# Kernel tuning notes

Measured on AMD Instinct MI355X. Metric: run time of the kernel, lower is better.

Reference implementation:

```python
import jax, jax.numpy as jnp
import numpy as np

NUM_HEADS = 16
D_MODEL = 1024
ROPE_THETA = 10000.0


def rope_cos_sin(H, W, head_dim, theta):
    # SAM2/SAM3 axial RoPE: first half of complex dims encode x, second half y.
    n = H * W
    t = jnp.arange(n)
    tx = (t % W).astype(jnp.float32)
    ty = (t // W).astype(jnp.float32)
    # freqs: 1 / theta^(arange(0, dim, 4)[:dim//4] / dim)
    exps = jnp.arange(0, head_dim, 4)[: head_dim // 4].astype(jnp.float32) / head_dim
    freqs = 1.0 / (theta ** exps)  # (head_dim//4,)
    ang = jnp.concatenate([tx[:, None] * freqs, ty[:, None] * freqs], axis=-1)  # (N, head_dim//2)
    return jnp.cos(ang), jnp.sin(ang)


def apply_rope(x, cos, sin):
    # x: (B, nh, N, D); pairs of features treated as complex numbers
    B, nh, N, D = x.shape
    xr = x.reshape(B, nh, N, D // 2, 2)
    xe, xo = xr[..., 0], xr[..., 1]
    oe = xe * cos - xo * sin
    oo = xe * sin + xo * cos
    return jnp.stack([oe, oo], axis=-1).reshape(B, nh, N, D)


def setup_inputs() -> dict:
    key = jax.random.key(0)
    ks = jax.random.split(key, 12)
    C = D_MODEL
    s = 1.0 / np.sqrt(C)
    inp = {
        "q": jax.random.normal(ks[0], (2, 2048, C), dtype=jnp.float32),
        "k": jax.random.normal(ks[1], (2, 2112, C), dtype=jnp.float32),
        "v": jax.random.normal(ks[2], (2, 2112, C), dtype=jnp.float32),
        "Wq": jax.random.normal(ks[3], (C, C), dtype=jnp.float32) * s,
        "bq": jax.random.normal(ks[4], (C,), dtype=jnp.float32) * s,
        "Wk": jax.random.normal(ks[5], (C, C), dtype=jnp.float32) * s,
        "bk": jax.random.normal(ks[6], (C,), dtype=jnp.float32) * s,
        "Wv": jax.random.normal(ks[7], (C, C), dtype=jnp.float32) * s,
        "bv": jax.random.normal(ks[8], (C,), dtype=jnp.float32) * s,
        "Wo": jax.random.normal(ks[9], (C, C), dtype=jnp.float32) * s,
        "bo": jax.random.normal(ks[10], (C,), dtype=jnp.float32) * s,
        "q_h": 32,
        "q_w": 64,
        "num_final_k_to_exclude": 64,
    }
    return inp


def reference(q, k, v, Wq, bq, Wk, bk, Wv, bv, Wo, bo, q_h, q_w, num_final_k_to_exclude):
    B, Nq, C = q.shape
    Nk = k.shape[1]
    nh = NUM_HEADS
    d = C // nh
    # QKV projections -> (B, nh, N, d)
    qh = (q @ Wq + bq).reshape(B, Nq, nh, d).transpose(0, 2, 1, 3)
    kh = (k @ Wk + bk).reshape(B, Nk, nh, d).transpose(0, 2, 1, 3)
    vh = (v @ Wv + bv).reshape(B, Nk, nh, d).transpose(0, 2, 1, 3)
    # RoPE on q and on first num_k_keep keys (exclude trailing pointer tokens)
    n_keep = Nk - num_final_k_to_exclude  # == q_h * q_w == Nq here
    cos, sin = rope_cos_sin(q_h, q_w, d, ROPE_THETA)
    qh = apply_rope(qh, cos, sin)
    k_rot = apply_rope(kh[:, :, :n_keep], cos, sin)
    kh = jnp.concatenate([k_rot, kh[:, :, n_keep:]], axis=2)
    # scaled dot-product attention
    scale = 1.0 / np.sqrt(d)
    scores = jnp.einsum("bhqd,bhkd->bhqk", qh, kh) * scale
    probs = jax.nn.softmax(scores, axis=-1)
    attn = jnp.einsum("bhqk,bhkd->bhqd", probs, vh)
    out = attn.transpose(0, 2, 1, 3).reshape(B, Nq, C)
    return out @ Wo + bo
```

## Files before the change

### kernel.cpp

```cpp
#include <hip/hip_runtime.h>

#define B_ 2
#define NQ 2048
#define NK 2112
#define CD 1024
#define NH 16
#define HD 64

typedef unsigned short u16;
typedef unsigned int u32;
typedef __attribute__((ext_vector_type(8))) __bf16 bf16x8;
typedef __attribute__((ext_vector_type(4))) float f32x4;

#define GPTR(p) ((const __attribute__((address_space(1))) void*)(p))
#define LPTR(p) ((__attribute__((address_space(3))) void*)(p))
#define GLL16(g, l) __builtin_amdgcn_global_load_lds(GPTR(g), LPTR(l), 16, 0, 0)

__device__ __forceinline__ u16 f2bf(float f) {
  u32 u = __float_as_uint(f);
  u32 r = u + 0x7fffu + ((u >> 16) & 1u);
  return (u16)(r >> 16);
}
__device__ __forceinline__ float bf2f(u16 h) { return __uint_as_float(((u32)h) << 16); }

__global__ void cvt3_kernel(const float* __restrict__ q, const float* __restrict__ k,
                            const float* __restrict__ v, u16* __restrict__ qb,
                            u16* __restrict__ kb, u16* __restrict__ vb) {
  int z = blockIdx.y;
  const float* src = (z == 0) ? q : (z == 1) ? k : v;
  u16* dst = (z == 0) ? qb : (z == 1) ? kb : vb;
  int n4 = (z == 0) ? (B_ * NQ * CD / 4) : (B_ * NK * CD / 4);
  int i = blockIdx.x * 256 + threadIdx.x;
  if (i >= n4) return;
  float4 vv = ((const float4*)src)[i];
  ushort4 o;
  o.x = f2bf(vv.x); o.y = f2bf(vv.y); o.z = f2bf(vv.z); o.w = f2bf(vv.w);
  ((ushort4*)dst)[i] = o;
}

__global__ void wtrans_kernel(const float* __restrict__ W0, const float* __restrict__ W1,
                              const float* __restrict__ W2, const float* __restrict__ W3,
                              u16* __restrict__ T0, u16* __restrict__ T1,
                              u16* __restrict__ T2, u16* __restrict__ T3) {
  const float* src; u16* dst;
  switch (blockIdx.z) {
    case 0: src = W0; dst = T0; break;
    case 1: src = W1; dst = T1; break;
    case 2: src = W2; dst = T2; break;
    default: src = W3; dst = T3; break;
  }
  __shared__ u16 tile[32][33];
  int t = threadIdx.x;
  int r0 = blockIdx.y * 32, c0 = blockIdx.x * 32;
  int row = t >> 3, c4 = (t & 7) * 4;
  float4 v = *(const float4*)&src[(r0 + row) * 1024 + c0 + c4];
  tile[row][c4 + 0] = f2bf(v.x);
  tile[row][c4 + 1] = f2bf(v.y);
  tile[row][c4 + 2] = f2bf(v.z);
  tile[row][c4 + 3] = f2bf(v.w);
  __syncthreads();
  ushort4 o;
  o.x = tile[c4 + 0][row];
  o.y = tile[c4 + 1][row];
  o.z = tile[c4 + 2][row];
  o.w = tile[c4 + 3][row];
  *(ushort4*)&dst[(c0 + row) * 1024 + r0 + c4] = o;
}

#define SC 0.18033688011112042f

__global__ __launch_bounds__(256, 2) void gemm_qkv(
    const u16* __restrict__ qb, const u16* __restrict__ kb, const u16* __restrict__ vb,
    const u16* __restrict__ wqt, const u16* __restrict__ wkt, const u16* __restrict__ wvt,
    const float* __restrict__ bq, const float* __restrict__ bk, const float* __restrict__ bv,
    u16* __restrict__ Qh, u16* __restrict__ Kh, u16* __restrict__ Vt) {
  const int z = blockIdx.z;
  if (z == 0 && blockIdx.y >= 32) return;
  const u16* A = (z == 0) ? qb : (z == 1) ? kb : vb;
  const u16* Bt = (z == 0) ? wqt : (z == 1) ? wkt : wvt;
  const float* bias = (z == 0) ? bq : (z == 1) ? bk : bv;
  const int batch_rows = (z == 0) ? NQ : NK;

  __shared__ u16 As[128 * 32];
  __shared__ u16 Bs[128 * 32];
  const int t = threadIdx.x;
  const int lane = t & 63, w = t >> 6;
  const int lc = lane & 15, lq = lane >> 4;
  const int m0 = blockIdx.y * 128, n0 = blockIdx.x * 128;
  const int wm = (w >> 1) * 64, wn = (w & 1) * 64;
  f32x4 acc[4][4] = {};
  const u16* ga = A + (m0 + (t >> 2)) * 1024 + (t & 3) * 8;
  const u16* gb = Bt + (n0 + (t >> 2)) * 1024 + (t & 3) * 8;
  char* lA = (char*)As + w * 1024;
  char* lB = (char*)Bs + w * 1024;
  for (int k0 = 0; k0 < 1024; k0 += 32) {
    if (k0) __syncthreads();
    GLL16(ga + k0, lA);
    GLL16(ga + 64 * 1024 + k0, lA + 4096);
    GLL16(gb + k0, lB);
    GLL16(gb + 64 * 1024 + k0, lB + 4096);
    __syncthreads();
    bf16x8 af[4], bf[4];
#pragma unroll
    for (int i = 0; i < 4; ++i) {
      af[i] = *(const bf16x8*)&As[(wm + i * 16 + lc) * 32 + lq * 8];
      bf[i] = *(const bf16x8*)&Bs[(wn + i * 16 + lc) * 32 + lq * 8];
    }
#pragma unroll
    for (int mi = 0; mi < 4; ++mi)
#pragma unroll
      for (int ni = 0; ni < 4; ++ni)
        acc[mi][ni] = __builtin_amdgcn_mfma_f32_16x16x32_bf16(af[mi], bf[ni], acc[mi][ni], 0, 0, 0);
  }
#pragma unroll
  for (int mi = 0; mi < 4; ++mi) {
#pragma unroll
    for (int ni = 0; ni < 4; ++ni) {
      int col = n0 + wn + ni * 16 + lc;
      float bv_ = bias[col];
      int j = (col >> 1) & 31;
      bool jlow = j < 16;
      float freq = exp2f((float)(jlow ? j : j - 16) * -0.8304820237f);
#pragma unroll
      for (int r = 0; r < 4; ++r) {
        int row = m0 + wm + mi * 16 + lq * 4 + r;
        float v = acc[mi][ni][r] + bv_;
        if (z < 2) {
          int bb = row >= batch_rows ? 1 : 0;
          int tok = row - bb * batch_rows;
          float p = __shfl_xor(v, 1, 64);
          float ov = v;
          if (tok < 2048) {
            float pos = jlow ? (float)(tok & 63) : (float)(tok >> 6);
            float s, c;
            __sincosf(pos * freq, &s, &c);
            ov = ((col & 1) == 0) ? (v * c - p * s) : (p * s + v * c);
          }
          if (z == 0) ov *= SC;
          ((z == 0) ? Qh : Kh)[row * 1024 + col] = f2bf(ov);
        } else {
          int bb = row >= NK ? 1 : 0;
          int tok = row - bb * NK;
          int h = col >> 6, dd = col & 63;
          Vt[((bb * NH + h) * HD + dd) * NK + tok] = f2bf(v);
        }
      }
    }
  }
}

__global__ __launch_bounds__(256, 2) void gemm_o(const u16* __restrict__ A,
                                                 const u16* __restrict__ Bt,
                                                 const float* __restrict__ bias,
                                                 float* __restrict__ Cout) {
  __shared__ u16 As[128 * 32];
  __shared__ u16 Bs[128 * 32];
  const int t = threadIdx.x;
  const int lane = t & 63, w = t >> 6;
  const int lc = lane & 15, lq = lane >> 4;
  const int m0 = blockIdx.y * 128, n0 = blockIdx.x * 128;
  const int wm = (w >> 1) * 64, wn = (w & 1) * 64;
  f32x4 acc[4][4] = {};
  const u16* ga = A + (m0 + (t >> 2)) * 1024 + (t & 3) * 8;
  const u16* gb = Bt + (n0 + (t >> 2)) * 1024 + (t & 3) * 8;
  char* lA = (char*)As + w * 1024;
  char* lB = (char*)Bs + w * 1024;
  for (int k0 = 0; k0 < 1024; k0 += 32) {
    if (k0) __syncthreads();
    GLL16(ga + k0, lA);
    GLL16(ga + 64 * 1024 + k0, lA + 4096);
    GLL16(gb + k0, lB);
    GLL16(gb + 64 * 1024 + k0, lB + 4096);
    __syncthreads();
    bf16x8 af[4], bf[4];
#pragma unroll
    for (int i = 0; i < 4; ++i) {
      af[i] = *(const bf16x8*)&As[(wm + i * 16 + lc) * 32 + lq * 8];
      bf[i] = *(const bf16x8*)&Bs[(wn + i * 16 + lc) * 32 + lq * 8];
    }
#pragma unroll
    for (int mi = 0; mi < 4; ++mi)
#pragma unroll
      for (int ni = 0; ni < 4; ++ni)
        acc[mi][ni] = __builtin_amdgcn_mfma_f32_16x16x32_bf16(af[mi], bf[ni], acc[mi][ni], 0, 0, 0);
  }
#pragma unroll
  for (int mi = 0; mi < 4; ++mi)
#pragma unroll
    for (int ni = 0; ni < 4; ++ni) {
      int col = n0 + wn + ni * 16 + lc;
      float bv = bias[col];
#pragma unroll
      for (int r = 0; r < 4; ++r) {
        int row = m0 + wm + mi * 16 + lq * 4 + r;
        Cout[row * 1024 + col] = acc[mi][ni][r] + bv;
      }
    }
}

#define LSTR 72
__global__ __launch_bounds__(256, 2) void attn_kernel(const u16* __restrict__ Qh,
                                                      const u16* __restrict__ Kh,
                                                      const u16* __restrict__ Vt,
                                                      u16* __restrict__ AO) {
  __shared__ u16 QPs[128 * LSTR];
  __shared__ u16 Ks[64 * LSTR];
  __shared__ u16 Vs[64 * LSTR];
  const int t = threadIdx.x;
  const int lane = t & 63, w = t >> 6;
  const int lc = lane & 15, lq = lane >> 4;
  const int rr = lane >> 3, s = lane & 7;
  const int qt = blockIdx.x, h = blockIdx.y, b = blockIdx.z;

  {
    const u16* gq = Qh + (b * NQ + qt * 128 + w * 32 + rr) * CD + h * HD + s * 8;
    u16* lqp = &QPs[(w * 32 + rr) * LSTR + s * 8];
#pragma unroll
    for (int i = 0; i < 4; ++i)
      *(uint4*)(lqp + i * 8 * LSTR) = *(const uint4*)(gq + i * 8 * CD);
  }
  bf16x8 qf[2][2];
#pragma unroll
  for (int ni = 0; ni < 2; ++ni)
#pragma unroll
    for (int kk = 0; kk < 2; ++kk)
      qf[ni][kk] = *(const bf16x8*)&QPs[(w * 32 + ni * 16 + lc) * LSTR + kk * 32 + lq * 8];

  bf16x8 ones;
  {
    u32* op = (u32*)&ones;
    op[0] = op[1] = op[2] = op[3] = 0x3F803F80u;
  }

  const u16* gK = Kh + (b * NK + w * 16 + rr) * CD + h * HD + s * 8;
  const u16* gV = Vt + ((b * NH + h) * HD + w * 16 + rr) * NK + s * 8;
  uint4 kreg0, kreg1, vreg0, vreg1;
  kreg0 = *(const uint4*)(gK);
  kreg1 = *(const uint4*)(gK + 8 * CD);
  vreg0 = *(const uint4*)(gV);
  vreg1 = *(const uint4*)(gV + 8 * NK);

  f32x4 oacc[2][4] = {};
  f32x4 lacc[2] = {};

  for (int j0 = 0; j0 < NK; j0 += 64) {
    __syncthreads();
    *(uint4*)&Ks[(w * 16 + rr) * LSTR + s * 8] = kreg0;
    *(uint4*)&Ks[(w * 16 + 8 + rr) * LSTR + s * 8] = kreg1;
    *(uint4*)&Vs[(w * 16 + rr) * LSTR + s * 8] = vreg0;
    *(uint4*)&Vs[(w * 16 + 8 + rr) * LSTR + s * 8] = vreg1;
    __syncthreads();
    if (j0 + 64 < NK) {
      kreg0 = *(const uint4*)(gK + (j0 + 64) * CD);
      kreg1 = *(const uint4*)(gK + (j0 + 64) * CD + 8 * CD);
      vreg0 = *(const uint4*)(gV + j0 + 64);
      vreg1 = *(const uint4*)(gV + 8 * NK + j0 + 64);
    }

    f32x4 st[2][4] = {};
#pragma unroll
    for (int mi = 0; mi < 4; ++mi) {
      bf16x8 k0f = *(const bf16x8*)&Ks[(mi * 16 + lc) * LSTR + lq * 8];
      bf16x8 k1f = *(const bf16x8*)&Ks[(mi * 16 + lc) * LSTR + 32 + lq * 8];
#pragma unroll
      for (int ni = 0; ni < 2; ++ni) {
        st[ni][mi] = __builtin_amdgcn_mfma_f32_16x16x32_bf16(k0f, qf[ni][0], st[ni][mi], 0, 0, 0);
        st[ni][mi] = __builtin_amdgcn_mfma_f32_16x16x32_bf16(k1f, qf[ni][1], st[ni][mi], 0, 0, 0);
      }
    }
#pragma unroll
    for (int ni = 0; ni < 2; ++ni)
#pragma unroll
      for (int mi = 0; mi < 4; ++mi) {
        u32 e0 = __float_as_uint(__builtin_amdgcn_exp2f(st[ni][mi][0])) + 0x8000u;
        u32 e1 = __float_as_uint(__builtin_amdgcn_exp2f(st[ni][mi][1])) + 0x8000u;
        u32 e2 = __float_as_uint(__builtin_amdgcn_exp2f(st[ni][mi][2])) + 0x8000u;
        u32 e3 = __float_as_uint(__builtin_amdgcn_exp2f(st[ni][mi][3])) + 0x8000u;
        uint2 pk;
        pk.x = __builtin_amdgcn_perm(e1, e0, 0x07060302u);
        pk.y = __builtin_amdgcn_perm(e3, e2, 0x07060302u);
        *(uint2*)&QPs[(w * 32 + ni * 16 + lc) * LSTR + mi * 16 + lq * 4] = pk;
      }
#pragma unroll
    for (int kc = 0; kc < 2; ++kc) {
      bf16x8 pf[2], vf[4];
#pragma unroll
      for (int ni = 0; ni < 2; ++ni)
        pf[ni] = *(const bf16x8*)&QPs[(w * 32 + ni * 16 + lc) * LSTR + kc * 32 + lq * 8];
#pragma unroll
      for (int di = 0; di < 4; ++di)
        vf[di] = *(const bf16x8*)&Vs[(di * 16 + lc) * LSTR + kc * 32 + lq * 8];
#pragma unroll
      for (int ni = 0; ni < 2; ++ni) {
#pragma unroll
        for (int di = 0; di < 4; ++di)
          oacc[ni][di] = __builtin_amdgcn_mfma_f32_16x16x32_bf16(pf[ni], vf[di], oacc[ni][di], 0, 0, 0);
        lacc[ni] = __builtin_amdgcn_mfma_f32_16x16x32_bf16(pf[ni], ones, lacc[ni], 0, 0, 0);
      }
    }
  }
#pragma unroll
  for (int ni = 0; ni < 2; ++ni)
#pragma unroll
    for (int r = 0; r < 4; ++r) {
      float inv = 1.0f / lacc[ni][r];
#pragma unroll
      for (int di = 0; di < 4; ++di) {
        int row = qt * 128 + w * 32 + ni * 16 + lq * 4 + r;
        int col = h * HD + di * 16 + lc;
        AO[(b * NQ + row) * CD + col] = f2bf(oacc[ni][di][r] * inv);
      }
    }
}

extern "C" void kernel_launch(void* const* d_in, const int* in_sizes, int n_in,
                              void* d_out, int out_size, void* d_ws, size_t ws_size,
                              hipStream_t stream) {
  const float* q  = (const float*)d_in[0];
  const float* k  = (const float*)d_in[1];
  const float* v  = (const float*)d_in[2];
  const float* Wq = (const float*)d_in[3];
  const float* bq = (const float*)d_in[4];
  const float* Wk = (const float*)d_in[5];
  const float* bk = (const float*)d_in[6];
  const float* Wv = (const float*)d_in[7];
  const float* bv = (const float*)d_in[8];
  const float* Wo = (const float*)d_in[9];
  const float* bo = (const float*)d_in[10];

  char* ws = (char*)d_ws;
  size_t off = 0;
  auto alloc = [&](size_t bytes) {
    char* p = ws + off;
    off += (bytes + 255) & ~(size_t)255;
    return p;
  };
  u16* qb  = (u16*)alloc((size_t)B_ * NQ * CD * 2);
  u16* kb  = (u16*)alloc((size_t)B_ * NK * CD * 2);
  u16* vb  = (u16*)alloc((size_t)B_ * NK * CD * 2);
  u16* wqt = (u16*)alloc((size_t)CD * CD * 2);
  u16* wkt = (u16*)alloc((size_t)CD * CD * 2);
  u16* wvt = (u16*)alloc((size_t)CD * CD * 2);
  u16* wot = (u16*)alloc((size_t)CD * CD * 2);
  u16* Qh  = (u16*)alloc((size_t)B_ * NQ * CD * 2);
  u16* Kh  = (u16*)alloc((size_t)B_ * NK * CD * 2);
  u16* Vt  = (u16*)alloc((size_t)B_ * NK * CD * 2);
  u16* AO  = (u16*)alloc((size_t)B_ * NQ * CD * 2);

  cvt3_kernel<<<dim3(4224, 3), 256, 0, stream>>>(q, k, v, qb, kb, vb);
  wtrans_kernel<<<dim3(32, 32, 4), 256, 0, stream>>>(Wq, Wk, Wv, Wo, wqt, wkt, wvt, wot);
  gemm_qkv<<<dim3(8, 33, 3), 256, 0, stream>>>(qb, kb, vb, wqt, wkt, wvt, bq, bk, bv, Qh, Kh, Vt);
  attn_kernel<<<dim3(16, NH, B_), 256, 0, stream>>>(Qh, Kh, Vt, AO);
  gemm_o<<<dim3(8, 32), 256, 0, stream>>>(AO, wot, bo, (float*)d_out);
}
```

Before: 262.9 us.

## Merge prep kernels, swap MFMA operands for vectorized epilogue stores, shrink O-proj tile

Fuses the activation conversion and weight transpose into one prep launch. In the Q/K projection it swaps the MFMA operands so each lane holds four consecutive columns, which lets the RoPE epilogue run without shuffles and write packed 8-byte stores. The V epilogue writes four consecutive tokens per store into the transposed layout. The output projection uses 128x64 tiles, doubling the grid, with float4 stores. This cuts launch overhead and scattered 2-byte writes, at the cost of more branching and a smaller per-block reuse in the O GEMM.

After: 261.3 us. About the same (-0.6%).

```diff
diff --git a/kernel.cpp b/kernel.cpp
--- a/kernel.cpp
+++ b/kernel.cpp
@@ -23,66 +23,67 @@
 }
 __device__ __forceinline__ float bf2f(u16 h) { return __uint_as_float(((u32)h) << 16); }
 
-__global__ void cvt3_kernel(const float* __restrict__ q, const float* __restrict__ k,
+#define SC 0.18033688011112042f
+#define NEGL2T 0.8304820237f
+#define FSTEP 0.5623413252f
+
+__global__ void prep_kernel(const float* __restrict__ q, const float* __restrict__ k,
                             const float* __restrict__ v, u16* __restrict__ qb,
-                            u16* __restrict__ kb, u16* __restrict__ vb) {
-  int z = blockIdx.y;
-  const float* src = (z == 0) ? q : (z == 1) ? k : v;
-  u16* dst = (z == 0) ? qb : (z == 1) ? kb : vb;
-  int n4 = (z == 0) ? (B_ * NQ * CD / 4) : (B_ * NK * CD / 4);
-  int i = blockIdx.x * 256 + threadIdx.x;
-  if (i >= n4) return;
-  float4 vv = ((const float4*)src)[i];
-  ushort4 o;
-  o.x = f2bf(vv.x); o.y = f2bf(vv.y); o.z = f2bf(vv.z); o.w = f2bf(vv.w);
-  ((ushort4*)dst)[i] = o;
-}
-
-__global__ void wtrans_kernel(const float* __restrict__ W0, const float* __restrict__ W1,
-                              const float* __restrict__ W2, const float* __restrict__ W3,
-                              u16* __restrict__ T0, u16* __restrict__ T1,
-                              u16* __restrict__ T2, u16* __restrict__ T3) {
-  const float* src; u16* dst;
-  switch (blockIdx.z) {
-    case 0: src = W0; dst = T0; break;
-    case 1: src = W1; dst = T1; break;
-    case 2: src = W2; dst = T2; break;
-    default: src = W3; dst = T3; break;
-  }
+                            u16* __restrict__ kb, u16* __restrict__ vb,
+                            const float* __restrict__ W0, const float* __restrict__ W1,
+                            const float* __restrict__ W2, const float* __restrict__ W3,
+                            u16* __restrict__ T0, u16* __restrict__ T1,
+                            u16* __restrict__ T2, u16* __restrict__ T3) {
   __shared__ u16 tile[32][33];
+  int y = blockIdx.y;
   int t = threadIdx.x;
-  int r0 = blockIdx.y * 32, c0 = blockIdx.x * 32;
-  int row = t >> 3, c4 = (t & 7) * 4;
-  float4 v = *(const float4*)&src[(r0 + row) * 1024 + c0 + c4];
-  tile[row][c4 + 0] = f2bf(v.x);
-  tile[row][c4 + 1] = f2bf(v.y);
-  tile[row][c4 + 2] = f2bf(v.z);
-  tile[row][c4 + 3] = f2bf(v.w);
-  __syncthreads();
-  ushort4 o;
-  o.x = tile[c4 + 0][row];
-  o.y = tile[c4 + 1][row];
-  o.z = tile[c4 + 2][row];
-  o.w = tile[c4 + 3][row];
-  *(ushort4*)&dst[(c0 + row) * 1024 + r0 + c4] = o;
-}
-
-#define SC 0.18033688011112042f
+  if (y < 3) {
+    const float* src = (y == 0) ? q : (y == 1) ? k : v;
+    u16* dst = (y == 0) ? qb : (y == 1) ? kb : vb;
+    int n4 = (y == 0) ? (B_ * NQ * CD / 4) : (B_ * NK * CD / 4);
+    int i = blockIdx.x * 256 + t;
+    if (i >= n4) return;
+    float4 vv = ((const float4*)src)[i];
+    ushort4 o;
+    o.x = f2bf(vv.x); o.y = f2bf(vv.y); o.z = f2bf(vv.z); o.w = f2bf(vv.w);
+    ((ushort4*)dst)[i] = o;
+  } else {
+    int x = blockIdx.x;
+    if (x >= 4096) return;
+    int which = x >> 10, xy = x & 1023;
+    const float* src = (which == 0) ? W0 : (which == 1) ? W1 : (which == 2) ? W2 : W3;
+    u16* dst = (which == 0) ? T0 : (which == 1) ? T1 : (which == 2) ? T2 : T3;
+    int r0 = (xy >> 5) * 32, c0 = (xy & 31) * 32;
+    int row = t >> 3, c4 = (t & 7) * 4;
+    float4 vv = *(const float4*)&src[(r0 + row) * 1024 + c0 + c4];
+    tile[row][c4 + 0] = f2bf(vv.x);
+    tile[row][c4 + 1] = f2bf(vv.y);
+    tile[row][c4 + 2] = f2bf(vv.z);
+    tile[row][c4 + 3] = f2bf(vv.w);
+    __syncthreads();
+    ushort4 o;
+    o.x = tile[c4 + 0][row];
+    o.y = tile[c4 + 1][row];
+    o.z = tile[c4 + 2][row];
+    o.w = tile[c4 + 3][row];
+    *(ushort4*)&dst[(c0 + row) * 1024 + r0 + c4] = o;
+  }
+}
 
 __global__ __launch_bounds__(256, 2) void gemm_qkv(
     const u16* __restrict__ qb, const u16* __restrict__ kb, const u16* __restrict__ vb,
     const u16* __restrict__ wqt, const u16* __restrict__ wkt, const u16* __restrict__ wvt,
     const float* __restrict__ bq, const float* __restrict__ bk, const float* __restrict__ bv,
     u16* __restrict__ Qh, u16* __restrict__ Kh, u16* __restrict__ Vt) {
+  __shared__ u16 As[128 * 32];
+  __shared__ u16 Bs[128 * 32];
   const int z = blockIdx.z;
   if (z == 0 && blockIdx.y >= 32) return;
   const u16* A = (z == 0) ? qb : (z == 1) ? kb : vb;
   const u16* Bt = (z == 0) ? wqt : (z == 1) ? wkt : wvt;
   const float* bias = (z == 0) ? bq : (z == 1) ? bk : bv;
-  const int batch_rows = (z == 0) ? NQ : NK;
-
-  __shared__ u16 As[128 * 32];
-  __shared__ u16 Bs[128 * 32];
+  const int BR = (z == 0) ? NQ : NK;
+
   const int t = threadIdx.x;
   const int lane = t & 63, w = t >> 6;
   const int lc = lane & 15, lq = lane >> 4;
@@ -93,6 +94,7 @@
   const u16* gb = Bt + (n0 + (t >> 2)) * 1024 + (t & 3) * 8;
   char* lA = (char*)As + w * 1024;
   char* lB = (char*)Bs + w * 1024;
+  const bool swap = (z < 2);
   for (int k0 = 0; k0 < 1024; k0 += 32) {
     if (k0) __syncthreads();
     GLL16(ga + k0, lA);
@@ -106,44 +108,78 @@
       af[i] = *(const bf16x8*)&As[(wm + i * 16 + lc) * 32 + lq * 8];
       bf[i] = *(const bf16x8*)&Bs[(wn + i * 16 + lc) * 32 + lq * 8];
     }
-#pragma unroll
-    for (int mi = 0; mi < 4; ++mi)
-#pragma unroll
-      for (int ni = 0; ni < 4; ++ni)
-        acc[mi][ni] = __builtin_amdgcn_mfma_f32_16x16x32_bf16(af[mi], bf[ni], acc[mi][ni], 0, 0, 0);
-  }
-#pragma unroll
-  for (int mi = 0; mi < 4; ++mi) {
+    if (swap) {
+#pragma unroll
+      for (int mi = 0; mi < 4; ++mi)
+#pragma unroll
+        for (int ni = 0; ni < 4; ++ni)
+          acc[mi][ni] = __builtin_amdgcn_mfma_f32_16x16x32_bf16(bf[ni], af[mi], acc[mi][ni], 0, 0, 0);
+    } else {
+#pragma unroll
+      for (int mi = 0; mi < 4; ++mi)
+#pragma unroll
+        for (int ni = 0; ni < 4; ++ni)
+          acc[mi][ni] = __builtin_amdgcn_mfma_f32_16x16x32_bf16(af[mi], bf[ni], acc[mi][ni], 0, 0, 0);
+    }
+  }
+
+  if (swap) {
+    u16* Out = (z == 0) ? Qh : Kh;
+    const bool isQ = (z == 0);
+#pragma unroll
+    for (int ni = 0; ni < 4; ++ni) {
+      int cb = n0 + wn + ni * 16 + lq * 4;
+      float4 bv4 = *(const float4*)&bias[cb];
+      int jj = (ni * 8 + lq * 2) & 15;
+      bool jl = ni < 2;
+      float f0 = exp2f((float)jj * -NEGL2T);
+      float f1 = f0 * FSTEP;
+#pragma unroll
+      for (int mi = 0; mi < 4; ++mi) {
+        int row = m0 + wm + mi * 16 + lc;
+        int bb = row >= BR ? 1 : 0;
+        int tok = row - bb * BR;
+        float v0 = acc[mi][ni][0] + bv4.x;
+        float v1 = acc[mi][ni][1] + bv4.y;
+        float v2 = acc[mi][ni][2] + bv4.z;
+        float v3 = acc[mi][ni][3] + bv4.w;
+        uint2 pk;
+        if (isQ || tok < 2048) {
+          float pos = jl ? (float)(tok & 63) : (float)(tok >> 6);
+          float s0, c0, s1, c1;
+          __sincosf(pos * f0, &s0, &c0);
+          __sincosf(pos * f1, &s1, &c1);
+          float o0 = v0 * c0 - v1 * s0, o1 = v0 * s0 + v1 * c0;
+          float o2 = v2 * c1 - v3 * s1, o3 = v2 * s1 + v3 * c1;
+          if (isQ) { o0 *= SC; o1 *= SC; o2 *= SC; o3 *= SC; }
+          pk.x = (u32)f2bf(o0) | ((u32)f2bf(o1) << 16);
+          pk.y = (u32)f2bf(o2) | ((u32)f2bf(o3) << 16);
+        } else {
+          pk.x = (u32)f2bf(v0) | ((u32)f2bf(v1) << 16);
+          pk.y = (u32)f2bf(v2) | ((u32)f2bf(v3) << 16);
+        }
+        *(uint2*)&Out[row * 1024 + cb] = pk;
+      }
+    }
+  } else {
 #pragma unroll
     for (int ni = 0; ni < 4; ++ni) {
       int col = n0 + wn + ni * 16 + lc;
-      float bv_ = bias[col];
-      int j = (col >> 1) & 31;
-      bool jlow = j < 16;
-      float freq = exp2f((float)(jlow ? j : j - 16) * -0.8304820237f);
-#pragma unroll
-      for (int r = 0; r < 4; ++r) {
-        int row = m0 + wm + mi * 16 + lq * 4 + r;
-        float v = acc[mi][ni][r] + bv_;
-        if (z < 2) {
-          int bb = row >= batch_rows ? 1 : 0;
-          int tok = row - bb * batch_rows;
-          float p = __shfl_xor(v, 1, 64);
-          float ov = v;
-          if (tok < 2048) {
-            float pos = jlow ? (float)(tok & 63) : (float)(tok >> 6);
-            float s, c;
-            __sincosf(pos * freq, &s, &c);
-            ov = ((col & 1) == 0) ? (v * c - p * s) : (p * s + v * c);
-          }
-          if (z == 0) ov *= SC;
-          ((z == 0) ? Qh : Kh)[row * 1024 + col] = f2bf(ov);
-        } else {
-          int bb = row >= NK ? 1 : 0;
-          int tok = row - bb * NK;
-          int h = col >> 6, dd = col & 63;
-          Vt[((bb * NH + h) * HD + dd) * NK + tok] = f2bf(v);
-        }
+      float bv = bias[col];
+      int hh = col >> 6, dd = col & 63;
+#pragma unroll
+      for (int mi = 0; mi < 4; ++mi) {
+        int row0 = m0 + wm + mi * 16 + lq * 4;
+        int bb = row0 >= NK ? 1 : 0;
+        int tok0 = row0 - bb * NK;
+        float v0 = acc[mi][ni][0] + bv;
+        float v1 = acc[mi][ni][1] + bv;
+        float v2 = acc[mi][ni][2] + bv;
+        float v3 = acc[mi][ni][3] + bv;
+        uint2 pk;
+        pk.x = (u32)f2bf(v0) | ((u32)f2bf(v1) << 16);
+        pk.y = (u32)f2bf(v2) | ((u32)f2bf(v3) << 16);
+        *(uint2*)&Vt[((bb * NH + hh) * HD + dd) * NK + tok0] = pk;
       }
     }
   }
@@ -154,13 +190,13 @@
                                                  const float* __restrict__ bias,
                                                  float* __restrict__ Cout) {
   __shared__ u16 As[128 * 32];
-  __shared__ u16 Bs[128 * 32];
+  __shared__ u16 Bs[64 * 32];
   const int t = threadIdx.x;
   const int lane = t & 63, w = t >> 6;
   const int lc = lane & 15, lq = lane >> 4;
-  const int m0 = blockIdx.y * 128, n0 = blockIdx.x * 128;
-  const int wm = (w >> 1) * 64, wn = (w & 1) * 64;
-  f32x4 acc[4][4] = {};
+  const int m0 = blockIdx.y * 128, n0 = blockIdx.x * 64;
+  const int wm = (w >> 1) * 64, wn = (w & 1) * 32;
+  f32x4 acc[4][2] = {};
   const u16* ga = A + (m0 + (t >> 2)) * 1024 + (t & 3) * 8;
   const u16* gb = Bt + (n0 + (t >> 2)) * 1024 + (t & 3) * 8;
   char* lA = (char*)As + w * 1024;
@@ -170,32 +206,35 @@
     GLL16(ga + k0, lA);
     GLL16(ga + 64 * 1024 + k0, lA + 4096);
     GLL16(gb + k0, lB);
-    GLL16(gb + 64 * 1024 + k0, lB + 4096);
-    __syncthreads();
-    bf16x8 af[4], bf[4];
-#pragma unroll
-    for (int i = 0; i < 4; ++i) {
+    __syncthreads();
+    bf16x8 af[4], bf[2];
+#pragma unroll
+    for (int i = 0; i < 4; ++i)
       af[i] = *(const bf16x8*)&As[(wm + i * 16 + lc) * 32 + lq * 8];
+#pragma unroll
+    for (int i = 0; i < 2; ++i)
       bf[i] = *(const bf16x8*)&Bs[(wn + i * 16 + lc) * 32 + lq * 8];
-    }
 #pragma unroll
     for (int mi = 0; mi < 4; ++mi)
 #pragma unroll
-      for (int ni = 0; ni < 4; ++ni)
-        acc[mi][ni] = __builtin_amdgcn_mfma_f32_16x16x32_bf16(af[mi], bf[ni], acc[mi][ni], 0, 0, 0);
-  }
-#pragma unroll
-  for (int mi = 0; mi < 4; ++mi)
-#pragma unroll
-    for (int ni = 0; ni < 4; ++ni) {
-      int col = n0 + wn + ni * 16 + lc;
-      float bv = bias[col];
-#pragma unroll
-      for (int r = 0; r < 4; ++r) {
-        int row = m0 + wm + mi * 16 + lq * 4 + r;
-        Cout[row * 1024 + col] = acc[mi][ni][r] + bv;
-      }
-    }
+      for (int ni = 0; ni < 2; ++ni)
+        acc[mi][ni] = __builtin_amdgcn_mfma_f32_16x16x32_bf16(bf[ni], af[mi], acc[mi][ni], 0, 0, 0);
+  }
+#pragma unroll
+  for (int ni = 0; ni < 2; ++ni) {
+    int cb = n0 + wn + ni * 16 + lq * 4;
+    float4 bv4 = *(const float4*)&bias[cb];
+#pragma unroll
+    for (int mi = 0; mi < 4; ++mi) {
+      int row = m0 + wm + mi * 16 + lc;
+      float4 o;
+      o.x = acc[mi][ni][0] + bv4.x;
+      o.y = acc[mi][ni][1] + bv4.y;
+      o.z = acc[mi][ni][2] + bv4.z;
+      o.w = acc[mi][ni][3] + bv4.w;
+      *(float4*)&Cout[row * 1024 + cb] = o;
+    }
+  }
 }
 
 #define LSTR 72
@@ -347,9 +386,9 @@
   u16* Vt  = (u16*)alloc((size_t)B_ * NK * CD * 2);
   u16* AO  = (u16*)alloc((size_t)B_ * NQ * CD * 2);
 
-  cvt3_kernel<<<dim3(4224, 3), 256, 0, stream>>>(q, k, v, qb, kb, vb);
-  wtrans_kernel<<<dim3(32, 32, 4), 256, 0, stream>>>(Wq, Wk, Wv, Wo, wqt, wkt, wvt, wot);
+  prep_kernel<<<dim3(4224, 4), 256, 0, stream>>>(q, k, v, qb, kb, vb,
+                                                 Wq, Wk, Wv, Wo, wqt, wkt, wvt, wot);
   gemm_qkv<<<dim3(8, 33, 3), 256, 0, stream>>>(qb, kb, vb, wqt, wkt, wvt, bq, bk, bv, Qh, Kh, Vt);
   attn_kernel<<<dim3(16, NH, B_), 256, 0, stream>>>(Qh, Kh, Vt, AO);
-  gemm_o<<<dim3(8, 32), 256, 0, stream>>>(AO, wot, bo, (float*)d_out);
-}
+  gemm_o<<<dim3(16, 32), 256, 0, stream>>>(AO, wot, bo, (float*)d_out);
+}
```
